# Optimization experiments

Hardware: AMD Instinct MI355X
Metric: run time of the kernel (lower is better)

## Reference

```python
import jax, jax.numpy as jnp
import numpy as np

H = 1024
V_IN = 32000
V_OUT = 32000
L = 256
START_ID = 1


def _gru_cell(x, h, Wi, Wh, bi, bh):
    # PyTorch GRU cell. x,h: [H]; Wi,Wh: [3H,H]; bi,bh: [3H]
    gi = Wi @ x + bi
    gh = Wh @ h + bh
    ir, iz, inn = jnp.split(gi, 3)
    hr, hz, hn = jnp.split(gh, 3)
    r = jax.nn.sigmoid(ir + hr)
    z = jax.nn.sigmoid(iz + hz)
    n = jnp.tanh(inn + r * hn)
    return (1.0 - z) * n + z * h


def setup_inputs() -> dict:
    key = jax.random.key(0)
    ks = jax.random.split(key, 20)
    s = 0.02
    d = {
        "input_ids": jax.random.randint(ks[0], (L,), 0, V_IN),
        "target_ids": jax.random.randint(ks[1], (L,), 0, V_OUT),
        "enc_emb": jax.random.normal(ks[2], (V_IN, H), jnp.float32) * s,
        "enc_Wi": jax.random.normal(ks[3], (3 * H, H), jnp.float32) * s,
        "enc_Wh": jax.random.normal(ks[4], (3 * H, H), jnp.float32) * s,
        "enc_bi": jnp.zeros((3 * H,), jnp.float32),
        "enc_bh": jnp.zeros((3 * H,), jnp.float32),
        "dec_emb": jax.random.normal(ks[5], (V_OUT, H), jnp.float32) * s,
        "dec_Wi": jax.random.normal(ks[6], (3 * H, H), jnp.float32) * s,
        "dec_Wh": jax.random.normal(ks[7], (3 * H, H), jnp.float32) * s,
        "dec_bi": jnp.zeros((3 * H,), jnp.float32),
        "dec_bh": jnp.zeros((3 * H,), jnp.float32),
        "attn_W": jax.random.normal(ks[8], (L, 2 * H), jnp.float32) * s,
        "attn_b": jnp.zeros((L,), jnp.float32),
        "comb_W": jax.random.normal(ks[9], (H, 2 * H), jnp.float32) * s,
        "comb_b": jnp.zeros((H,), jnp.float32),
        "out_W": jax.random.normal(ks[10], (V_OUT, H), jnp.float32) * s,
        "out_b": jnp.zeros((V_OUT,), jnp.float32),
    }
    return d


def reference(input_ids, target_ids, enc_emb, enc_Wi, enc_Wh, enc_bi, enc_bh,
              dec_emb, dec_Wi, dec_Wh, dec_bi, dec_bh,
              attn_W, attn_b, comb_W, comb_b, out_W, out_b):
    # ---- encoder: per-step GRU over input tokens, batch=1 ----
    enc_x = enc_emb[input_ids]  # [L, H]

    def enc_step(h, x):
        h2 = _gru_cell(x, h, enc_Wi, enc_Wh, enc_bi, enc_bh)
        return h2, h2

    h0 = jnp.zeros((H,), enc_emb.dtype)
    enc_hidden, enc_outs = jax.lax.scan(enc_step, h0, enc_x)  # enc_outs: [L, H]

    # ---- decoder with teacher forcing (deterministic branch) ----
    dec_in_ids = jnp.concatenate([jnp.array([START_ID], input_ids.dtype), target_ids[:-1]])

    def dec_step(h, inp):
        tok, tgt = inp
        e = dec_emb[tok]  # [H] (dropout in eval mode = identity)
        scores = attn_W @ jnp.concatenate([e, h]) + attn_b  # [L]
        a = jax.nn.softmax(scores)
        ctx = a @ enc_outs  # [H]
        c = jax.nn.relu(comb_W @ jnp.concatenate([e, ctx]) + comb_b)
        h2 = _gru_cell(c, h, dec_Wi, dec_Wh, dec_bi, dec_bh)
        logp = jax.nn.log_softmax(out_W @ h2 + out_b)  # [V_OUT]
        return h2, -logp[tgt]

    _, nll = jax.lax.scan(dec_step, enc_hidden, (dec_in_ids, target_ids))
    return jnp.sum(nll)
```

## Files before the change

### kernel.cpp

```cpp
#include <hip/hip_runtime.h>
#include <math.h>

#define H 1024
#define SEQ 256
#define VOUT 32000

__device__ __forceinline__ float sigmoidf_(float x) { return 1.f / (1.f + expf(-x)); }

__device__ __forceinline__ float cload(const float* p) {
    return __hip_atomic_load(p, __ATOMIC_RELAXED, __HIP_MEMORY_SCOPE_AGENT);
}
__device__ __forceinline__ void cstore(float* p, float v) {
    __hip_atomic_store(p, v, __ATOMIC_RELAXED, __HIP_MEMORY_SCOPE_AGENT);
}

__device__ __forceinline__ void gbar(int* bar, int target) {
    __syncthreads();
    if (threadIdx.x == 0) {
        int* leaf = bar + ((blockIdx.x & 15) << 4);
        int a = __hip_atomic_fetch_add(leaf, 1, __ATOMIC_RELAXED, __HIP_MEMORY_SCOPE_AGENT);
        if (a == 16 * target - 1) {
            int r = __hip_atomic_fetch_add(bar + 320, 1, __ATOMIC_RELAXED, __HIP_MEMORY_SCOPE_AGENT);
            if (r == 16 * target - 1) {
                __hip_atomic_store(bar + 384, target, __ATOMIC_RELAXED, __HIP_MEMORY_SCOPE_AGENT);
            }
        }
        while (__hip_atomic_load(bar + 384, __ATOMIC_RELAXED, __HIP_MEMORY_SCOPE_AGENT) < target) {
            __builtin_amdgcn_s_sleep(2);
        }
    }
    __syncthreads();
}

__global__ __launch_bounds__(256) void gather_kernel(
    const int* __restrict__ input_ids, const int* __restrict__ target_ids,
    const float* __restrict__ enc_emb, const float* __restrict__ dec_emb,
    float* __restrict__ enc_x, float* __restrict__ dec_e)
{
    int b = blockIdx.x, tid = threadIdx.x;
    if (b < SEQ) {
        int tok = input_ids[b];
        const float4* src = (const float4*)(enc_emb + (size_t)tok * H);
        float4* dst = (float4*)(enc_x + (size_t)b * H);
        dst[tid] = src[tid];
    } else {
        int t = b - SEQ;
        int tok = (t == 0) ? 1 : target_ids[t - 1];
        const float4* src = (const float4*)(dec_emb + (size_t)tok * H);
        float4* dst = (float4*)(dec_e + (size_t)t * H);
        dst[tid] = src[tid];
    }
}

__global__ __launch_bounds__(256) void init_kernel(float* __restrict__ hbuf,
                                                   int* __restrict__ bar)
{
    int i = blockIdx.x * 256 + threadIdx.x;
    if (i < 2 * H) hbuf[i] = 0.f;
    if (i < 1024) bar[i] = 0;
}

__global__ __launch_bounds__(256) void gemm_nt_kernel(
    const float* __restrict__ A, const float* __restrict__ B,
    const float* __restrict__ bias, float* __restrict__ C,
    int Kdim, int lda, int offa, int ldb, int ldc)
{
    __shared__ float As[16][68];
    __shared__ float Bs[16][68];
    const int tid = threadIdx.x;
    const int m0 = blockIdx.y * 64;
    const int n0 = blockIdx.x * 64;
    const int tr = (tid >> 4) << 2;
    const int tc = (tid & 15) << 2;
    const int lrow = tid >> 2;
    const int lk = (tid & 3) << 2;
    const float* Ab = A + (size_t)m0 * lda + offa;
    const float* Bb = B + (size_t)n0 * ldb;
    float acc[4][4] = {{0.f,0.f,0.f,0.f},{0.f,0.f,0.f,0.f},{0.f,0.f,0.f,0.f},{0.f,0.f,0.f,0.f}};

    for (int k0 = 0; k0 < Kdim; k0 += 16) {
        float4 av = *(const float4*)(Ab + (size_t)lrow * lda + (k0 + lk));
        float4 bv = *(const float4*)(Bb + (size_t)lrow * ldb + (k0 + lk));
        As[lk + 0][lrow] = av.x; As[lk + 1][lrow] = av.y;
        As[lk + 2][lrow] = av.z; As[lk + 3][lrow] = av.w;
        Bs[lk + 0][lrow] = bv.x; Bs[lk + 1][lrow] = bv.y;
        Bs[lk + 2][lrow] = bv.z; Bs[lk + 3][lrow] = bv.w;
        __syncthreads();
#pragma unroll
        for (int k = 0; k < 16; ++k) {
            float4 a = *(const float4*)(&As[k][tr]);
            float4 b = *(const float4*)(&Bs[k][tc]);
            acc[0][0] = fmaf(a.x, b.x, acc[0][0]);
            acc[0][1] = fmaf(a.x, b.y, acc[0][1]);
            acc[0][2] = fmaf(a.x, b.z, acc[0][2]);
            acc[0][3] = fmaf(a.x, b.w, acc[0][3]);
            acc[1][0] = fmaf(a.y, b.x, acc[1][0]);
            acc[1][1] = fmaf(a.y, b.y, acc[1][1]);
            acc[1][2] = fmaf(a.y, b.z, acc[1][2]);
            acc[1][3] = fmaf(a.y, b.w, acc[1][3]);
            acc[2][0] = fmaf(a.z, b.x, acc[2][0]);
            acc[2][1] = fmaf(a.z, b.y, acc[2][1]);
            acc[2][2] = fmaf(a.z, b.z, acc[2][2]);
            acc[2][3] = fmaf(a.z, b.w, acc[2][3]);
            acc[3][0] = fmaf(a.w, b.x, acc[3][0]);
            acc[3][1] = fmaf(a.w, b.y, acc[3][1]);
            acc[3][2] = fmaf(a.w, b.z, acc[3][2]);
            acc[3][3] = fmaf(a.w, b.w, acc[3][3]);
        }
        __syncthreads();
    }
#pragma unroll
    for (int i = 0; i < 4; ++i) {
#pragma unroll
        for (int j = 0; j < 4; ++j) {
            float v = acc[i][j];
            if (bias) v += bias[n0 + tc + j];
            C[(size_t)(m0 + tr + i) * ldc + (n0 + tc + j)] = v;
        }
    }
}

__global__ __launch_bounds__(256, 1) void enc_rnn_kernel(
    const float* __restrict__ Wh, const float* __restrict__ bh,
    const float* __restrict__ gi_all,
    float* __restrict__ hbuf, float* __restrict__ encH, int* __restrict__ bar)
{
    __shared__ float h_s[H];
    const int tid = threadIdx.x;
    const int wave = tid >> 6, lane = tid & 63;
    const int u = blockIdx.x * 4 + wave;

    float rWr[16], rWz[16], rWn[16];
    {
        const float* wr = Wh + (size_t)u * H;
        const float* wz = Wh + (size_t)(u + H) * H;
        const float* wn = Wh + (size_t)(u + 2 * H) * H;
#pragma unroll
        for (int i = 0; i < 16; ++i) {
            int k = lane + (i << 6);
            rWr[i] = wr[k]; rWz[i] = wz[k]; rWn[i] = wn[k];
        }
    }
    const float bhr = bh[u], bhz = bh[H + u], bhn = bh[2 * H + u];

    for (int t = 0; t < SEQ; ++t) {
        const float* h = hbuf + (t & 1) * H;
        float* hnext = hbuf + ((t + 1) & 1) * H;
        const float g0 = gi_all[t * 3 * H + u];
        const float g1 = gi_all[t * 3 * H + H + u];
        const float g2 = gi_all[t * 3 * H + 2 * H + u];

        for (int i = tid; i < H; i += 256) h_s[i] = cload(h + i);
        __syncthreads();

        float dr = 0.f, dz = 0.f, dn = 0.f;
#pragma unroll
        for (int i = 0; i < 16; ++i) {
            float hv = h_s[lane + (i << 6)];
            dr = fmaf(rWr[i], hv, dr);
            dz = fmaf(rWz[i], hv, dz);
            dn = fmaf(rWn[i], hv, dn);
        }
#pragma unroll
        for (int off = 32; off > 0; off >>= 1) {
            dr += __shfl_down(dr, off);
            dz += __shfl_down(dz, off);
            dn += __shfl_down(dn, off);
        }
        if (lane == 0) {
            float r = sigmoidf_(g0 + dr + bhr);
            float z = sigmoidf_(g1 + dz + bhz);
            float n = tanhf(g2 + r * (dn + bhn));
            float h2 = (1.f - z) * n + z * h_s[u];
            cstore(hnext + u, h2);
            encH[(size_t)t * H + u] = h2;
        }
        gbar(bar, t + 1);
    }
}

__global__ __launch_bounds__(256, 1) void dec_rnn_kernel(
    const float* __restrict__ attn_W, const float* __restrict__ attn_e,
    const float* __restrict__ M, const float* __restrict__ comb_pre,
    const float* __restrict__ Wi, const float* __restrict__ Wh,
    const float* __restrict__ bi, const float* __restrict__ bh,
    float* __restrict__ hbuf, float* __restrict__ s_g,
    float* __restrict__ c_g, float* __restrict__ hs_dec, int* __restrict__ bar)
{
    __shared__ float h_s[H];
    __shared__ float c_s[H];
    __shared__ float a_s[SEQ];
    __shared__ float red4[4];
    const int b = blockIdx.x, tid = threadIdx.x;
    const int wave = tid >> 6, lane = tid & 63;
    const int u = b * 4 + wave;

    float rWir[16], rWiz[16], rWin[16], rWhr[16], rWhz[16], rWhn[16];
    {
        const float* wir = Wi + (size_t)u * H;
        const float* wiz = Wi + (size_t)(u + H) * H;
        const float* win = Wi + (size_t)(u + 2 * H) * H;
        const float* whr = Wh + (size_t)u * H;
        const float* whz = Wh + (size_t)(u + H) * H;
        const float* whn = Wh + (size_t)(u + 2 * H) * H;
#pragma unroll
        for (int i = 0; i < 16; ++i) {
            int k = lane + (i << 6);
            rWir[i] = wir[k]; rWiz[i] = wiz[k]; rWin[i] = win[k];
            rWhr[i] = whr[k]; rWhz[i] = whz[k]; rWhn[i] = whn[k];
        }
    }
    float rA[4];
    {
        const float* arow = attn_W + (size_t)b * (2 * H) + H;
#pragma unroll
        for (int j = 0; j < 4; ++j) rA[j] = arow[tid + (j << 8)];
    }
    float rM[4];
    {
        const float* Mrow = M + (size_t)u * SEQ;
#pragma unroll
        for (int j = 0; j < 4; ++j) rM[j] = Mrow[lane + (j << 6)];
    }
    const float bir = bi[u], biz = bi[H + u], bin_ = bi[2 * H + u];
    const float bhr = bh[u], bhz = bh[H + u], bhn = bh[2 * H + u];

    for (int t = 0; t < SEQ; ++t) {
        const float* h = hbuf + (t & 1) * H;
        float* hnext = hbuf + ((t + 1) & 1) * H;
        const float aev  = attn_e[t * SEQ + b];
        const float cpre = comb_pre[t * H + u];

        float hr0 = cload(h + tid);
        float hr1 = cload(h + tid + 256);
        float hr2 = cload(h + tid + 512);
        float hr3 = cload(h + tid + 768);
        h_s[tid]       = hr0;
        h_s[tid + 256] = hr1;
        h_s[tid + 512] = hr2;
        h_s[tid + 768] = hr3;

        float p = fmaf(rA[0], hr0, 0.f);
        p = fmaf(rA[1], hr1, p);
        p = fmaf(rA[2], hr2, p);
        p = fmaf(rA[3], hr3, p);
#pragma unroll
        for (int off = 32; off > 0; off >>= 1) p += __shfl_down(p, off);
        if (lane == 0) red4[wave] = p;
        __syncthreads();
        if (tid == 0)
            cstore(s_g + b, red4[0] + red4[1] + red4[2] + red4[3] + aev);
        gbar(bar, 3 * t + 1);

        float sv = cload(s_g + tid);
        float m = sv;
#pragma unroll
        for (int off = 32; off > 0; off >>= 1) m = fmaxf(m, __shfl_down(m, off));
        if (lane == 0) red4[wave] = m;
        __syncthreads();
        float mx = fmaxf(fmaxf(red4[0], red4[1]), fmaxf(red4[2], red4[3]));
        float ev = expf(sv - mx);
        a_s[tid] = ev;
        float ssum = ev;
#pragma unroll
        for (int off = 32; off > 0; off >>= 1) ssum += __shfl_down(ssum, off);
        __syncthreads();
        if (lane == 0) red4[wave] = ssum;
        __syncthreads();
        float inv = 1.f / (red4[0] + red4[1] + red4[2] + red4[3]);
        float pc = fmaf(a_s[lane], rM[0], 0.f);
        pc = fmaf(a_s[lane + 64],  rM[1], pc);
        pc = fmaf(a_s[lane + 128], rM[2], pc);
        pc = fmaf(a_s[lane + 192], rM[3], pc);
#pragma unroll
        for (int off = 32; off > 0; off >>= 1) pc += __shfl_down(pc, off);
        if (lane == 0)
            cstore(c_g + u, fmaxf(0.f, cpre + pc * inv));
        gbar(bar, 3 * t + 2);

        c_s[tid]       = cload(c_g + tid);
        c_s[tid + 256] = cload(c_g + tid + 256);
        c_s[tid + 512] = cload(c_g + tid + 512);
        c_s[tid + 768] = cload(c_g + tid + 768);
        __syncthreads();
        float dir = 0.f, diz = 0.f, din = 0.f, dhr = 0.f, dhz = 0.f, dhn = 0.f;
#pragma unroll
        for (int i = 0; i < 16; ++i) {
            int k = lane + (i << 6);
            float cv = c_s[k], hv = h_s[k];
            dir = fmaf(rWir[i], cv, dir);
            diz = fmaf(rWiz[i], cv, diz);
            din = fmaf(rWin[i], cv, din);
            dhr = fmaf(rWhr[i], hv, dhr);
            dhz = fmaf(rWhz[i], hv, dhz);
            dhn = fmaf(rWhn[i], hv, dhn);
        }
#pragma unroll
        for (int off = 32; off > 0; off >>= 1) {
            dir += __shfl_down(dir, off); diz += __shfl_down(diz, off);
            din += __shfl_down(din, off); dhr += __shfl_down(dhr, off);
            dhz += __shfl_down(dhz, off); dhn += __shfl_down(dhn, off);
        }
        if (lane == 0) {
            float r = sigmoidf_(dir + bir + dhr + bhr);
            float z = sigmoidf_(diz + biz + dhz + bhz);
            float n = tanhf(din + bin_ + r * (dhn + bhn));
            float h2 = (1.f - z) * n + z * h_s[u];
            cstore(hnext + u, h2);
            hs_dec[(size_t)t * H + u] = h2;
        }
        gbar(bar, 3 * t + 3);
    }
}

__global__ __launch_bounds__(256) void nll_kernel(
    const float* __restrict__ logits, const int* __restrict__ target_ids,
    float* __restrict__ nll)
{
    const int t = blockIdx.x, tid = threadIdx.x;
    __shared__ float red[256];
    const float* row = logits + (size_t)t * VOUT;
    float mx = -1e30f;
    for (int i = tid; i < VOUT; i += 256) mx = fmaxf(mx, row[i]);
    red[tid] = mx;
    __syncthreads();
    for (int off = 128; off > 0; off >>= 1) {
        if (tid < off) red[tid] = fmaxf(red[tid], red[tid + off]);
        __syncthreads();
    }
    mx = red[0];
    __syncthreads();
    float s = 0.f;
    for (int i = tid; i < VOUT; i += 256) s += expf(row[i] - mx);
    red[tid] = s;
    __syncthreads();
    for (int off = 128; off > 0; off >>= 1) {
        if (tid < off) red[tid] += red[tid + off];
        __syncthreads();
    }
    if (tid == 0) {
        float lse = mx + logf(red[0]);
        nll[t] = lse - row[target_ids[t]];
    }
}

__global__ __launch_bounds__(256) void sum_kernel(
    const float* __restrict__ nll, float* __restrict__ out)
{
    __shared__ float red[256];
    int tid = threadIdx.x;
    red[tid] = nll[tid];
    __syncthreads();
    for (int off = 128; off > 0; off >>= 1) {
        if (tid < off) red[tid] += red[tid + off];
        __syncthreads();
    }
    if (tid == 0) out[0] = red[0];
}

extern "C" void kernel_launch(void* const* d_in, const int* in_sizes, int n_in,
                              void* d_out, int out_size, void* d_ws, size_t ws_size,
                              hipStream_t stream)
{
    const int*   input_ids  = (const int*)d_in[0];
    const int*   target_ids = (const int*)d_in[1];
    const float* enc_emb = (const float*)d_in[2];
    const float* enc_Wi  = (const float*)d_in[3];
    const float* enc_Wh  = (const float*)d_in[4];
    const float* enc_bi  = (const float*)d_in[5];
    const float* enc_bh  = (const float*)d_in[6];
    const float* dec_emb = (const float*)d_in[7];
    const float* dec_Wi  = (const float*)d_in[8];
    const float* dec_Wh  = (const float*)d_in[9];
    const float* dec_bi  = (const float*)d_in[10];
    const float* dec_bh  = (const float*)d_in[11];
    const float* attn_W  = (const float*)d_in[12];
    const float* attn_b  = (const float*)d_in[13];
    const float* comb_W  = (const float*)d_in[14];
    const float* comb_b  = (const float*)d_in[15];
    const float* out_W   = (const float*)d_in[16];
    const float* out_b   = (const float*)d_in[17];
    float* out = (float*)d_out;

    float* ws = (float*)d_ws;
    float* enc_x    = ws; ws += SEQ * H;
    float* dec_e    = ws; ws += SEQ * H;
    float* enc_gi   = ws; ws += SEQ * 3 * H;
    float* attn_e   = ws; ws += SEQ * SEQ;
    float* comb_pre = ws; ws += SEQ * H;
    float* Mmat     = ws; ws += H * SEQ;
    float* encH     = ws; ws += SEQ * H;
    float* hs_dec   = ws; ws += SEQ * H;
    float* hbuf     = ws; ws += 2 * H;
    float* s_g      = ws; ws += SEQ;
    float* c_g      = ws; ws += H;
    float* nll      = ws; ws += SEQ;
    int*   bar_all  = (int*)ws; ws += 1024;
    ws += (256 - ((ws - (float*)d_ws) & 255)) & 255;
    float* logits   = ws; ws += (size_t)SEQ * VOUT;

    int* bar_enc = bar_all;
    int* bar_dec = bar_all + 512;

    hipLaunchKernelGGL(gather_kernel, dim3(512), dim3(256), 0, stream,
                       input_ids, target_ids, enc_emb, dec_emb, enc_x, dec_e);
    hipLaunchKernelGGL(init_kernel, dim3(16), dim3(256), 0, stream, hbuf, bar_all);

    hipLaunchKernelGGL(gemm_nt_kernel, dim3(3 * H / 64, SEQ / 64), dim3(256), 0, stream,
                       enc_x, enc_Wi, enc_bi, enc_gi, H, H, 0, H, 3 * H);
    hipLaunchKernelGGL(gemm_nt_kernel, dim3(SEQ / 64, SEQ / 64), dim3(256), 0, stream,
                       dec_e, attn_W, attn_b, attn_e, H, H, 0, 2 * H, SEQ);
    hipLaunchKernelGGL(gemm_nt_kernel, dim3(H / 64, SEQ / 64), dim3(256), 0, stream,
                       dec_e, comb_W, comb_b, comb_pre, H, H, 0, 2 * H, H);

    {
        void* args[] = {(void*)&enc_Wh, (void*)&enc_bh, (void*)&enc_gi,
                        (void*)&hbuf, (void*)&encH, (void*)&bar_enc};
        hipLaunchCooperativeKernel((void*)enc_rnn_kernel, dim3(256), dim3(256),
                                   args, 0, stream);
    }

    hipLaunchKernelGGL(gemm_nt_kernel, dim3(SEQ / 64, H / 64), dim3(256), 0, stream,
                       comb_W, encH, (const float*)nullptr, Mmat, H, 2 * H, H, H, SEQ);

    {
        void* args[] = {(void*)&attn_W, (void*)&attn_e, (void*)&Mmat, (void*)&comb_pre,
                        (void*)&dec_Wi, (void*)&dec_Wh, (void*)&dec_bi, (void*)&dec_bh,
                        (void*)&hbuf, (void*)&s_g, (void*)&c_g, (void*)&hs_dec,
                        (void*)&bar_dec};
        hipLaunchCooperativeKernel((void*)dec_rnn_kernel, dim3(256), dim3(256),
                                   args, 0, stream);
    }

    hipLaunchKernelGGL(gemm_nt_kernel, dim3(VOUT / 64, SEQ / 64), dim3(256), 0, stream,
                       hs_dec, out_W, out_b, logits, H, H, 0, H, VOUT);

    hipLaunchKernelGGL(nll_kernel, dim3(SEQ), dim3(256), 0, stream,
                       logits, target_ids, nll);
    hipLaunchKernelGGL(sum_kernel, dim3(1), dim3(256), 0, stream, nll, out);
}
```

Measured before the change: 4.353 ms.

## Replace grid barriers with tagged 64-bit value flags in RNN kernels

Removes the hierarchical atomic grid barrier from the encoder and decoder recurrent kernels. Each published value (hidden state, attention score, context) is now packed with a step tag into a 64-bit atomic word, and consumers spin until every value they need carries the expected tag. This turns a global barrier into point-to-point dataflow waits, and double-buffered shared memory keeps one step's reads from racing the next step's writes. The cost is twice the memory traffic per value and more polling loads. Correctness now rests on the tag protocol, including the encoder's final tag matching the decoder's starting tag.

```diff
diff --git a/kernel.cpp b/kernel.cpp
--- a/kernel.cpp
+++ b/kernel.cpp
@@ -5,31 +5,38 @@
 #define SEQ 256
 #define VOUT 32000
 
+typedef unsigned long long u64;
+
 __device__ __forceinline__ float sigmoidf_(float x) { return 1.f / (1.f + expf(-x)); }
 
-__device__ __forceinline__ float cload(const float* p) {
+__device__ __forceinline__ u64 aload64(const u64* p) {
     return __hip_atomic_load(p, __ATOMIC_RELAXED, __HIP_MEMORY_SCOPE_AGENT);
 }
-__device__ __forceinline__ void cstore(float* p, float v) {
-    __hip_atomic_store(p, v, __ATOMIC_RELAXED, __HIP_MEMORY_SCOPE_AGENT);
-}
-
-__device__ __forceinline__ void gbar(int* bar, int target) {
-    __syncthreads();
-    if (threadIdx.x == 0) {
-        int* leaf = bar + ((blockIdx.x & 15) << 4);
-        int a = __hip_atomic_fetch_add(leaf, 1, __ATOMIC_RELAXED, __HIP_MEMORY_SCOPE_AGENT);
-        if (a == 16 * target - 1) {
-            int r = __hip_atomic_fetch_add(bar + 320, 1, __ATOMIC_RELAXED, __HIP_MEMORY_SCOPE_AGENT);
-            if (r == 16 * target - 1) {
-                __hip_atomic_store(bar + 384, target, __ATOMIC_RELAXED, __HIP_MEMORY_SCOPE_AGENT);
-            }
-        }
-        while (__hip_atomic_load(bar + 384, __ATOMIC_RELAXED, __HIP_MEMORY_SCOPE_AGENT) < target) {
-            __builtin_amdgcn_s_sleep(2);
-        }
-    }
-    __syncthreads();
+__device__ __forceinline__ void publish(u64* p, float v, unsigned tag) {
+    u64 pk = ((u64)tag << 32) | (u64)__float_as_uint(v);
+    __hip_atomic_store(p, pk, __ATOMIC_RELAXED, __HIP_MEMORY_SCOPE_AGENT);
+}
+__device__ __forceinline__ float wait1(const u64* p, unsigned tag) {
+    u64 v = aload64(p);
+    while ((unsigned)(v >> 32) != tag) {
+        __builtin_amdgcn_s_sleep(1);
+        v = aload64(p);
+    }
+    return __uint_as_float((unsigned)v);
+}
+__device__ __forceinline__ void wait4(const u64* p0, const u64* p1,
+                                      const u64* p2, const u64* p3, unsigned tag,
+                                      float& o0, float& o1, float& o2, float& o3) {
+    u64 v0 = aload64(p0), v1 = aload64(p1), v2 = aload64(p2), v3 = aload64(p3);
+    while ((unsigned)(v0 >> 32) != tag || (unsigned)(v1 >> 32) != tag ||
+           (unsigned)(v2 >> 32) != tag || (unsigned)(v3 >> 32) != tag) {
+        __builtin_amdgcn_s_sleep(1);
+        v0 = aload64(p0); v1 = aload64(p1); v2 = aload64(p2); v3 = aload64(p3);
+    }
+    o0 = __uint_as_float((unsigned)v0);
+    o1 = __uint_as_float((unsigned)v1);
+    o2 = __uint_as_float((unsigned)v2);
+    o3 = __uint_as_float((unsigned)v3);
 }
 
 __global__ __launch_bounds__(256) void gather_kernel(
@@ -52,12 +59,10 @@
     }
 }
 
-__global__ __launch_bounds__(256) void init_kernel(float* __restrict__ hbuf,
-                                                   int* __restrict__ bar)
+__global__ __launch_bounds__(256) void init_kernel(u64* __restrict__ h64)
 {
     int i = blockIdx.x * 256 + threadIdx.x;
-    if (i < 2 * H) hbuf[i] = 0.f;
-    if (i < 1024) bar[i] = 0;
+    if (i < 2 * H) h64[i] = 0ULL;
 }
 
 __global__ __launch_bounds__(256) void gemm_nt_kernel(
@@ -123,9 +128,9 @@
 __global__ __launch_bounds__(256, 1) void enc_rnn_kernel(
     const float* __restrict__ Wh, const float* __restrict__ bh,
     const float* __restrict__ gi_all,
-    float* __restrict__ hbuf, float* __restrict__ encH, int* __restrict__ bar)
-{
-    __shared__ float h_s[H];
+    u64* __restrict__ h64, float* __restrict__ encH)
+{
+    __shared__ float h_s[2][H];
     const int tid = threadIdx.x;
     const int wave = tid >> 6, lane = tid & 63;
     const int u = blockIdx.x * 4 + wave;
@@ -144,19 +149,25 @@
     const float bhr = bh[u], bhz = bh[H + u], bhn = bh[2 * H + u];
 
     for (int t = 0; t < SEQ; ++t) {
-        const float* h = hbuf + (t & 1) * H;
-        float* hnext = hbuf + ((t + 1) & 1) * H;
+        const int p = t & 1;
         const float g0 = gi_all[t * 3 * H + u];
         const float g1 = gi_all[t * 3 * H + H + u];
         const float g2 = gi_all[t * 3 * H + 2 * H + u];
 
-        for (int i = tid; i < H; i += 256) h_s[i] = cload(h + i);
+        u64* hs = h64 + p * H;
+        float f0, f1, f2, f3;
+        wait4(hs + tid, hs + tid + 256, hs + tid + 512, hs + tid + 768,
+              (unsigned)t, f0, f1, f2, f3);
+        h_s[p][tid]       = f0;
+        h_s[p][tid + 256] = f1;
+        h_s[p][tid + 512] = f2;
+        h_s[p][tid + 768] = f3;
         __syncthreads();
 
         float dr = 0.f, dz = 0.f, dn = 0.f;
 #pragma unroll
         for (int i = 0; i < 16; ++i) {
-            float hv = h_s[lane + (i << 6)];
+            float hv = h_s[p][lane + (i << 6)];
             dr = fmaf(rWr[i], hv, dr);
             dz = fmaf(rWz[i], hv, dz);
             dn = fmaf(rWn[i], hv, dn);
@@ -171,11 +182,10 @@
             float r = sigmoidf_(g0 + dr + bhr);
             float z = sigmoidf_(g1 + dz + bhz);
             float n = tanhf(g2 + r * (dn + bhn));
-            float h2 = (1.f - z) * n + z * h_s[u];
-            cstore(hnext + u, h2);
+            float h2 = (1.f - z) * n + z * h_s[p][u];
+            publish(h64 + ((t + 1) & 1) * H + u, h2, (unsigned)(t + 1));
             encH[(size_t)t * H + u] = h2;
         }
-        gbar(bar, t + 1);
     }
 }
 
@@ -184,13 +194,14 @@
     const float* __restrict__ M, const float* __restrict__ comb_pre,
     const float* __restrict__ Wi, const float* __restrict__ Wh,
     const float* __restrict__ bi, const float* __restrict__ bh,
-    float* __restrict__ hbuf, float* __restrict__ s_g,
-    float* __restrict__ c_g, float* __restrict__ hs_dec, int* __restrict__ bar)
-{
-    __shared__ float h_s[H];
+    u64* __restrict__ h64, u64* __restrict__ s64,
+    u64* __restrict__ c64, float* __restrict__ hs_dec)
+{
+    __shared__ float h_s[2][H];
     __shared__ float c_s[H];
     __shared__ float a_s[SEQ];
     __shared__ float red4[4];
+    __shared__ float red4b[4];
     const int b = blockIdx.x, tid = threadIdx.x;
     const int wave = tid >> 6, lane = tid & 63;
     const int u = b * 4 + wave;
@@ -226,48 +237,48 @@
     const float bhr = bh[u], bhz = bh[H + u], bhn = bh[2 * H + u];
 
     for (int t = 0; t < SEQ; ++t) {
-        const float* h = hbuf + (t & 1) * H;
-        float* hnext = hbuf + ((t + 1) & 1) * H;
+        const int p = t & 1;
+        const unsigned htag = (unsigned)(SEQ + t);
+        const unsigned stag = (unsigned)(t + 1);
         const float aev  = attn_e[t * SEQ + b];
         const float cpre = comb_pre[t * H + u];
 
-        float hr0 = cload(h + tid);
-        float hr1 = cload(h + tid + 256);
-        float hr2 = cload(h + tid + 512);
-        float hr3 = cload(h + tid + 768);
-        h_s[tid]       = hr0;
-        h_s[tid + 256] = hr1;
-        h_s[tid + 512] = hr2;
-        h_s[tid + 768] = hr3;
-
-        float p = fmaf(rA[0], hr0, 0.f);
-        p = fmaf(rA[1], hr1, p);
-        p = fmaf(rA[2], hr2, p);
-        p = fmaf(rA[3], hr3, p);
-#pragma unroll
-        for (int off = 32; off > 0; off >>= 1) p += __shfl_down(p, off);
-        if (lane == 0) red4[wave] = p;
+        u64* hs = h64 + p * H;
+        float hr0, hr1, hr2, hr3;
+        wait4(hs + tid, hs + tid + 256, hs + tid + 512, hs + tid + 768,
+              htag, hr0, hr1, hr2, hr3);
+        h_s[p][tid]       = hr0;
+        h_s[p][tid + 256] = hr1;
+        h_s[p][tid + 512] = hr2;
+        h_s[p][tid + 768] = hr3;
+
+        float pp = fmaf(rA[0], hr0, 0.f);
+        pp = fmaf(rA[1], hr1, pp);
+        pp = fmaf(rA[2], hr2, pp);
+        pp = fmaf(rA[3], hr3, pp);
+#pragma unroll
+        for (int off = 32; off > 0; off >>= 1) pp += __shfl_down(pp, off);
+        if (lane == 0) red4[wave] = pp;
         __syncthreads();
         if (tid == 0)
-            cstore(s_g + b, red4[0] + red4[1] + red4[2] + red4[3] + aev);
-        gbar(bar, 3 * t + 1);
-
-        float sv = cload(s_g + tid);
+            publish(s64 + b, red4[0] + red4[1] + red4[2] + red4[3] + aev, stag);
+
+        float sv = wait1(s64 + tid, stag);
         float m = sv;
 #pragma unroll
         for (int off = 32; off > 0; off >>= 1) m = fmaxf(m, __shfl_down(m, off));
-        if (lane == 0) red4[wave] = m;
-        __syncthreads();
-        float mx = fmaxf(fmaxf(red4[0], red4[1]), fmaxf(red4[2], red4[3]));
+        if (lane == 0) red4b[wave] = m;
+        __syncthreads();
+        float mx = fmaxf(fmaxf(red4b[0], red4b[1]), fmaxf(red4b[2], red4b[3]));
         float ev = expf(sv - mx);
         a_s[tid] = ev;
         float ssum = ev;
 #pragma unroll
         for (int off = 32; off > 0; off >>= 1) ssum += __shfl_down(ssum, off);
         __syncthreads();
-        if (lane == 0) red4[wave] = ssum;
-        __syncthreads();
-        float inv = 1.f / (red4[0] + red4[1] + red4[2] + red4[3]);
+        if (lane == 0) red4b[wave] = ssum;
+        __syncthreads();
+        float inv = 1.f / (red4b[0] + red4b[1] + red4b[2] + red4b[3]);
         float pc = fmaf(a_s[lane], rM[0], 0.f);
         pc = fmaf(a_s[lane + 64],  rM[1], pc);
         pc = fmaf(a_s[lane + 128], rM[2], pc);
@@ -275,19 +286,21 @@
 #pragma unroll
         for (int off = 32; off > 0; off >>= 1) pc += __shfl_down(pc, off);
         if (lane == 0)
-            cstore(c_g + u, fmaxf(0.f, cpre + pc * inv));
-        gbar(bar, 3 * t + 2);
-
-        c_s[tid]       = cload(c_g + tid);
-        c_s[tid + 256] = cload(c_g + tid + 256);
-        c_s[tid + 512] = cload(c_g + tid + 512);
-        c_s[tid + 768] = cload(c_g + tid + 768);
+            publish(c64 + u, fmaxf(0.f, cpre + pc * inv), stag);
+
+        float c0, c1, c2, c3;
+        wait4(c64 + tid, c64 + tid + 256, c64 + tid + 512, c64 + tid + 768,
+              stag, c0, c1, c2, c3);
+        c_s[tid]       = c0;
+        c_s[tid + 256] = c1;
+        c_s[tid + 512] = c2;
+        c_s[tid + 768] = c3;
         __syncthreads();
         float dir = 0.f, diz = 0.f, din = 0.f, dhr = 0.f, dhz = 0.f, dhn = 0.f;
 #pragma unroll
         for (int i = 0; i < 16; ++i) {
             int k = lane + (i << 6);
-            float cv = c_s[k], hv = h_s[k];
+            float cv = c_s[k], hv = h_s[p][k];
             dir = fmaf(rWir[i], cv, dir);
             diz = fmaf(rWiz[i], cv, diz);
             din = fmaf(rWin[i], cv, din);
@@ -305,11 +318,10 @@
             float r = sigmoidf_(dir + bir + dhr + bhr);
             float z = sigmoidf_(diz + biz + dhz + bhz);
             float n = tanhf(din + bin_ + r * (dhn + bhn));
-            float h2 = (1.f - z) * n + z * h_s[u];
-            cstore(hnext + u, h2);
+            float h2 = (1.f - z) * n + z * h_s[p][u];
+            publish(h64 + ((t + 1) & 1) * H + u, h2, htag + 1);
             hs_dec[(size_t)t * H + u] = h2;
         }
-        gbar(bar, 3 * t + 3);
     }
 }
 
@@ -391,20 +403,16 @@
     float* Mmat     = ws; ws += H * SEQ;
     float* encH     = ws; ws += SEQ * H;
     float* hs_dec   = ws; ws += SEQ * H;
-    float* hbuf     = ws; ws += 2 * H;
-    float* s_g      = ws; ws += SEQ;
-    float* c_g      = ws; ws += H;
+    u64*   h64      = (u64*)ws; ws += 2 * H * 2;
+    u64*   s64      = (u64*)ws; ws += SEQ * 2;
+    u64*   c64      = (u64*)ws; ws += H * 2;
     float* nll      = ws; ws += SEQ;
-    int*   bar_all  = (int*)ws; ws += 1024;
     ws += (256 - ((ws - (float*)d_ws) & 255)) & 255;
     float* logits   = ws; ws += (size_t)SEQ * VOUT;
 
-    int* bar_enc = bar_all;
-    int* bar_dec = bar_all + 512;
-
     hipLaunchKernelGGL(gather_kernel, dim3(512), dim3(256), 0, stream,
                        input_ids, target_ids, enc_emb, dec_emb, enc_x, dec_e);
-    hipLaunchKernelGGL(init_kernel, dim3(16), dim3(256), 0, stream, hbuf, bar_all);
+    hipLaunchKernelGGL(init_kernel, dim3(8), dim3(256), 0, stream, h64);
 
     hipLaunchKernelGGL(gemm_nt_kernel, dim3(3 * H / 64, SEQ / 64), dim3(256), 0, stream,
                        enc_x, enc_Wi, enc_bi, enc_gi, H, H, 0, H, 3 * H);
@@ -415,7 +423,7 @@
 
     {
         void* args[] = {(void*)&enc_Wh, (void*)&enc_bh, (void*)&enc_gi,
-                        (void*)&hbuf, (void*)&encH, (void*)&bar_enc};
+                        (void*)&h64, (void*)&encH};
         hipLaunchCooperativeKernel((void*)enc_rnn_kernel, dim3(256), dim3(256),
                                    args, 0, stream);
     }
@@ -426,8 +434,7 @@
     {
         void* args[] = {(void*)&attn_W, (void*)&attn_e, (void*)&Mmat, (void*)&comb_pre,
                         (void*)&dec_Wi, (void*)&dec_Wh, (void*)&dec_bi, (void*)&dec_bh,
-                        (void*)&hbuf, (void*)&s_g, (void*)&c_g, (void*)&hs_dec,
-                        (void*)&bar_dec};
+                        (void*)&h64, (void*)&s64, (void*)&c64, (void*)&hs_dec};
         hipLaunchCooperativeKernel((void*)dec_rnn_kernel, dim3(256), dim3(256),
                                    args, 0, stream);
     }
```

After: 4.688 ms. 7.7% more time.
